# Kernel tuning notes

Measured on AMD Instinct MI355X. Metric: run time of the kernel, lower is better.

Reference implementation:

```python
import jax, jax.numpy as jnp
import numpy as np

W_IMG = 512
H_IMG = 512
D_MODEL = 192
N_FREQ = 8
LN_EPS = 1e-5


def _fourier_pe(coords_norm):
    # coords_norm: [B,K,2] in [0,1); returns [B,K,4*N_FREQ]
    freqs = 2.0 ** jnp.arange(N_FREQ, dtype=jnp.float32)  # [F]
    two_pi = 2.0 * jnp.pi
    x = coords_norm[..., 0:1] * freqs * two_pi  # [B,K,F]
    y = coords_norm[..., 1:2] * freqs * two_pi
    return jnp.concatenate([jnp.sin(x), jnp.cos(x), jnp.sin(y), jnp.cos(y)], axis=-1)


def _bilinear_sample(feat, gx, gy):
    # feat: [B,C,H,W]; gx,gy: [B,K] normalized coords in [-1,1], align_corners=True
    B, C, H, W = feat.shape
    ix = (gx + 1.0) * 0.5 * (W - 1)
    iy = (gy + 1.0) * 0.5 * (H - 1)
    ix0 = jnp.floor(ix)
    iy0 = jnp.floor(iy)
    wx = ix - ix0  # [B,K]
    wy = iy - iy0
    x0 = jnp.clip(ix0.astype(jnp.int32), 0, W - 1)
    x1 = jnp.clip(ix0.astype(jnp.int32) + 1, 0, W - 1)
    y0 = jnp.clip(iy0.astype(jnp.int32), 0, H - 1)
    y1 = jnp.clip(iy0.astype(jnp.int32) + 1, 0, H - 1)
    b = jnp.arange(B)[:, None]  # [B,1] broadcast against [B,K]
    g = lambda y, x: feat[b, :, y, x]  # [B,K,C]
    out = (g(y0, x0) * ((1 - wx) * (1 - wy))[..., None]
           + g(y0, x1) * (wx * (1 - wy))[..., None]
           + g(y1, x0) * ((1 - wx) * wy)[..., None]
           + g(y1, x1) * (wx * wy)[..., None])
    return out  # [B,K,C]


def setup_inputs() -> dict:
    key = jax.random.key(0)
    ks = jax.random.split(key, 16)
    B, K = 8, 4096
    # pixel coordinates in [0, W_IMG-1] x [0, H_IMG-1]
    u = jax.random.uniform(ks[0], (B, K, 2), dtype=jnp.float32)
    coords = u * jnp.array([W_IMG - 1, H_IMG - 1], dtype=jnp.float32)
    L1 = jax.random.normal(ks[1], (B, D_MODEL, 128, 128), dtype=jnp.float32)
    L2 = jax.random.normal(ks[2], (B, D_MODEL, 64, 64), dtype=jnp.float32)
    L3 = jax.random.normal(ks[3], (B, D_MODEL, 32, 32), dtype=jnp.float32)
    L4 = jax.random.normal(ks[4], (B, D_MODEL, 16, 16), dtype=jnp.float32)
    d_in = D_MODEL * 4 + 4 * N_FREQ  # 800
    Wseed_w = jax.random.normal(ks[5], (D_MODEL, d_in), dtype=jnp.float32) / np.sqrt(d_in)
    Wseed_b = jnp.zeros((D_MODEL,), dtype=jnp.float32)
    ln_g = jnp.ones((D_MODEL,), dtype=jnp.float32)
    ln_b = jnp.zeros((D_MODEL,), dtype=jnp.float32)
    Wpos_w = jax.random.normal(ks[6], (D_MODEL, 4 * N_FREQ), dtype=jnp.float32) / np.sqrt(4 * N_FREQ)
    Wpos_b = jnp.zeros((D_MODEL,), dtype=jnp.float32)
    return {"coords": coords, "L1": L1, "L2": L2, "L3": L3, "L4": L4,
            "Wseed_w": Wseed_w, "Wseed_b": Wseed_b, "ln_g": ln_g, "ln_b": ln_b,
            "Wpos_w": Wpos_w, "Wpos_b": Wpos_b}


def reference(coords, L1, L2, L3, L4, Wseed_w, Wseed_b, ln_g, ln_b, Wpos_w, Wpos_b):
    B, K, _ = coords.shape
    # normalized grid in [-1,1] (x uses W, y uses H), align_corners=True convention
    gx = 2.0 * coords[..., 0] / (W_IMG - 1) - 1.0  # [B,K]
    gy = 2.0 * coords[..., 1] / (H_IMG - 1) - 1.0
    center_grid = jnp.stack([gx, gy], axis=-1).reshape(B, K, 1, 2)
    coords_norm = coords / jnp.array([W_IMG, H_IMG], dtype=jnp.float32)
    pe_q = _fourier_pe(coords_norm)  # [B,K,32]
    f1 = _bilinear_sample(L1, gx, gy)
    f2 = _bilinear_sample(L2, gx, gy)
    f3 = _bilinear_sample(L3, gx, gy)
    f4 = _bilinear_sample(L4, gx, gy)
    x = jnp.concatenate([f1, f2, f3, f4, pe_q], axis=-1)  # [B,K,800]
    seed = x @ Wseed_w.T + Wseed_b
    mu = jnp.mean(seed, axis=-1, keepdims=True)
    var = jnp.mean((seed - mu) ** 2, axis=-1, keepdims=True)
    seed = (seed - mu) / jnp.sqrt(var + LN_EPS) * ln_g + ln_b
    pos = pe_q @ Wpos_w.T + Wpos_b
    return (seed, pos, center_grid)
```

## Files before the change

kernel.cpp:

```cpp
#include <hip/hip_runtime.h>
#include <stdint.h>

typedef unsigned short u16;
typedef short s16x8 __attribute__((ext_vector_type(8)));
typedef float f32x4 __attribute__((ext_vector_type(4)));

__device__ __forceinline__ u16 f2bf(float f) {
  union { float f; uint32_t u; } a; a.f = f;
  uint32_t u = a.u;
  uint32_t r = (u + 0x7fffu + ((u >> 16) & 1u)) >> 16;
  return (u16)r;
}
__device__ __forceinline__ float bf2f(uint32_t hbits) {
  union { uint32_t u; float f; } a; a.u = hbits << 16;
  return a.f;
}

__global__ void convert_w_kernel(const float* __restrict__ ws_w,
                                 const float* __restrict__ wp_w,
                                 u16* __restrict__ dst_ws, u16* __restrict__ dst_wp) {
  int i = blockIdx.x * 256 + threadIdx.x;
  if (i < 153600) dst_ws[i] = f2bf(ws_w[i]);
  if (i < 6144)   dst_wp[i] = f2bf(wp_w[i]);
}

__global__ __launch_bounds__(256) void transpose_kernel(const float* __restrict__ src,
                                                        u16* __restrict__ dst, int HW) {
  __shared__ u16 tile[192][66];
  const int b = blockIdx.y;
  const int hw0 = blockIdx.x * 64;
  const int t = threadIdx.x;
  const float* s = src + (size_t)b * 192 * HW + hw0;
  for (int i = 0; i < 48; ++i) {
    int idx = i * 256 + t;
    int c = idx >> 6, hw = idx & 63;
    tile[c][hw] = f2bf(s[(size_t)c * HW + hw]);
  }
  __syncthreads();
  uint32_t* d = (uint32_t*)(dst + ((size_t)b * HW + hw0) * 192);
  for (int i = 0; i < 24; ++i) {
    int e = i * 256 + t;
    int hw = e / 96, c2 = e - hw * 96;
    uint32_t v = (uint32_t)tile[c2 * 2][hw] | ((uint32_t)tile[c2 * 2 + 1][hw] << 16);
    d[hw * 96 + c2] = v;
  }
}

__global__ __launch_bounds__(256, 2) void seed_main(
    const float* __restrict__ coords,
    const u16* __restrict__ T1, const u16* __restrict__ T2,
    const u16* __restrict__ T3, const u16* __restrict__ T4,
    const u16* __restrict__ Wseed, const u16* __restrict__ Wpos,
    const float* __restrict__ seed_b, const float* __restrict__ ln_g,
    const float* __restrict__ ln_b, const float* __restrict__ pos_b,
    float* __restrict__ out_seed, float* __restrict__ out_pos,
    float* __restrict__ out_cg) {

  __shared__ __align__(16) u16 xt[32 * 808];
  __shared__ int   coff[32][4][4];
  __shared__ float cw[32][4][4];
  __shared__ float mu_s[32], rs_s[32];

  const int t = threadIdx.x;
  const int gp0 = blockIdx.x * 32;
  const int b = gp0 >> 12;

  if (t < 128) {
    int p = t >> 2, lv = t & 3;
    float cx = coords[(gp0 + p) * 2 + 0];
    float cy = coords[(gp0 + p) * 2 + 1];
    float gx = 2.0f * cx / 511.0f - 1.0f;
    float gy = 2.0f * cy / 511.0f - 1.0f;
    if (lv == 0) {
      out_cg[(gp0 + p) * 2 + 0] = gx;
      out_cg[(gp0 + p) * 2 + 1] = gy;
    }
    int Wl = 128 >> lv;
    float ix = (gx + 1.0f) * 0.5f * (float)(Wl - 1);
    float iy = (gy + 1.0f) * 0.5f * (float)(Wl - 1);
    float fx = floorf(ix), fy = floorf(iy);
    float wx = ix - fx, wy = iy - fy;
    int x0 = (int)fx, y0 = (int)fy;
    int x1 = x0 + 1, y1 = y0 + 1;
    x0 = min(max(x0, 0), Wl - 1); x1 = min(max(x1, 0), Wl - 1);
    y0 = min(max(y0, 0), Wl - 1); y1 = min(max(y1, 0), Wl - 1);
    coff[p][lv][0] = (y0 * Wl + x0) * 192;
    coff[p][lv][1] = (y0 * Wl + x1) * 192;
    coff[p][lv][2] = (y1 * Wl + x0) * 192;
    coff[p][lv][3] = (y1 * Wl + x1) * 192;
    cw[p][lv][0] = (1.0f - wx) * (1.0f - wy);
    cw[p][lv][1] = wx * (1.0f - wy);
    cw[p][lv][2] = (1.0f - wx) * wy;
    cw[p][lv][3] = wx * wy;
  }
  for (int i = 0; i < 4; ++i) {
    int e = i * 256 + t;
    int p = e >> 5, j = e & 31;
    float c = coords[(gp0 + p) * 2 + ((j >> 4) & 1)] * (1.0f / 512.0f);
    float v = c * (float)(1 << (j & 7));
    float a = (v - floorf(v)) * 6.283185307179586f;
    float r = (j & 8) ? cosf(a) : sinf(a);
    xt[p * 808 + 768 + j] = f2bf(r);
  }
  __syncthreads();

  const size_t psz1 = (size_t)16384 * 192, psz2 = (size_t)4096 * 192,
               psz3 = (size_t)1024 * 192,  psz4 = (size_t)256 * 192;
  const u16* B1 = T1 + (size_t)b * psz1;
  const u16* B2 = T2 + (size_t)b * psz2;
  const u16* B3 = T3 + (size_t)b * psz3;
  const u16* B4 = T4 + (size_t)b * psz4;
  for (int i = 0; i < 48; ++i) {
    int e = i * 256 + t;
    int c2 = e % 96;
    int plv = e / 96;
    int lv = plv & 3, p = plv >> 2;
    const u16* base = (lv == 0) ? B1 : (lv == 1) ? B2 : (lv == 2) ? B3 : B4;
    float w0 = cw[p][lv][0], w1 = cw[p][lv][1], w2 = cw[p][lv][2], w3 = cw[p][lv][3];
    int cc = c2 * 2;
    uint32_t u0 = *(const uint32_t*)(base + coff[p][lv][0] + cc);
    uint32_t u1 = *(const uint32_t*)(base + coff[p][lv][1] + cc);
    uint32_t u2 = *(const uint32_t*)(base + coff[p][lv][2] + cc);
    uint32_t u3 = *(const uint32_t*)(base + coff[p][lv][3] + cc);
    float lo = bf2f(u0 & 0xffff) * w0 + bf2f(u1 & 0xffff) * w1 +
               bf2f(u2 & 0xffff) * w2 + bf2f(u3 & 0xffff) * w3;
    float hi = bf2f(u0 >> 16) * w0 + bf2f(u1 >> 16) * w1 +
               bf2f(u2 >> 16) * w2 + bf2f(u3 >> 16) * w3;
    uint32_t pv = (uint32_t)f2bf(lo) | ((uint32_t)f2bf(hi) << 16);
    *(uint32_t*)(xt + p * 808 + lv * 192 + cc) = pv;
  }
  __syncthreads();

  const int wv = t >> 6, lid = t & 63;
  const int quad = lid >> 4, mrow = lid & 15;
  const int nt0 = wv * 3;

  f32x4 accS[2][3], accP[2][3];
#pragma unroll
  for (int mt = 0; mt < 2; ++mt)
#pragma unroll
    for (int j = 0; j < 3; ++j) { accS[mt][j] = (f32x4)0.0f; accP[mt][j] = (f32x4)0.0f; }

  s16x8 a_last[2];
#pragma unroll 1
  for (int kc = 0; kc < 25; ++kc) {
    int ko = kc * 32 + quad * 8;
    s16x8 a0 = *(const s16x8*)(xt + mrow * 808 + ko);
    s16x8 a1 = *(const s16x8*)(xt + (16 + mrow) * 808 + ko);
#pragma unroll
    for (int j = 0; j < 3; ++j) {
      int n = (nt0 + j) * 16 + mrow;
      s16x8 bw = *(const s16x8*)(Wseed + n * 800 + ko);
      accS[0][j] = __builtin_amdgcn_mfma_f32_16x16x32_bf16(a0, bw, accS[0][j], 0, 0, 0);
      accS[1][j] = __builtin_amdgcn_mfma_f32_16x16x32_bf16(a1, bw, accS[1][j], 0, 0, 0);
    }
    if (kc == 24) { a_last[0] = a0; a_last[1] = a1; }
  }
#pragma unroll
  for (int j = 0; j < 3; ++j) {
    int n = (nt0 + j) * 16 + mrow;
    s16x8 bw = *(const s16x8*)(Wpos + n * 32 + quad * 8);
    accP[0][j] = __builtin_amdgcn_mfma_f32_16x16x32_bf16(a_last[0], bw, accP[0][j], 0, 0, 0);
    accP[1][j] = __builtin_amdgcn_mfma_f32_16x16x32_bf16(a_last[1], bw, accP[1][j], 0, 0, 0);
  }

#pragma unroll
  for (int j = 0; j < 3; ++j) {
    int n = (nt0 + j) * 16 + mrow;
    float pb = pos_b[n];
#pragma unroll
    for (int mt = 0; mt < 2; ++mt)
#pragma unroll
      for (int r = 0; r < 4; ++r) {
        int row = gp0 + mt * 16 + quad * 4 + r;
        out_pos[(size_t)row * 192 + n] = accP[mt][j][r] + pb;
      }
  }

  __syncthreads();
  float* preLN = (float*)xt;
#pragma unroll
  for (int j = 0; j < 3; ++j) {
    int n = (nt0 + j) * 16 + mrow;
    float sb = seed_b[n];
#pragma unroll
    for (int mt = 0; mt < 2; ++mt)
#pragma unroll
      for (int r = 0; r < 4; ++r)
        preLN[(mt * 16 + quad * 4 + r) * 193 + n] = accS[mt][j][r] + sb;
  }
  __syncthreads();

  {
    int r = t >> 3, g = t & 7;
    float s = 0.0f, sq = 0.0f;
    for (int i = 0; i < 24; ++i) {
      float v = preLN[r * 193 + g * 24 + i];
      s += v; sq += v * v;
    }
    for (int d = 4; d > 0; d >>= 1) {
      s += __shfl_down(s, d, 8);
      sq += __shfl_down(sq, d, 8);
    }
    if (g == 0) {
      float mu = s * (1.0f / 192.0f);
      float var = sq * (1.0f / 192.0f) - mu * mu;
      mu_s[r] = mu;
      rs_s[r] = 1.0f / sqrtf(var + 1e-5f);
    }
  }
  __syncthreads();

  for (int i = 0; i < 24; ++i) {
    int e = i * 256 + t;
    int r = e / 192, n = e - r * 192;
    float v = (preLN[r * 193 + n] - mu_s[r]) * rs_s[r] * ln_g[n] + ln_b[n];
    out_seed[(size_t)(gp0 + r) * 192 + n] = v;
  }
}

extern "C" void kernel_launch(void* const* d_in, const int* in_sizes, int n_in,
                              void* d_out, int out_size, void* d_ws, size_t ws_size,
                              hipStream_t stream) {
  const float* coords  = (const float*)d_in[0];
  const float* L1      = (const float*)d_in[1];
  const float* L2      = (const float*)d_in[2];
  const float* L3      = (const float*)d_in[3];
  const float* L4      = (const float*)d_in[4];
  const float* Wseed_w = (const float*)d_in[5];
  const float* Wseed_b = (const float*)d_in[6];
  const float* ln_g    = (const float*)d_in[7];
  const float* ln_b    = (const float*)d_in[8];
  const float* Wpos_w  = (const float*)d_in[9];
  const float* Wpos_b  = (const float*)d_in[10];

  u16* T1  = (u16*)d_ws;
  u16* T2  = T1 + (size_t)8 * 16384 * 192;
  u16* T3  = T2 + (size_t)8 * 4096 * 192;
  u16* T4  = T3 + (size_t)8 * 1024 * 192;
  u16* Wsd = T4 + (size_t)8 * 256 * 192;
  u16* Wps = Wsd + 153600;

  convert_w_kernel<<<600, 256, 0, stream>>>(Wseed_w, Wpos_w, Wsd, Wps);
  transpose_kernel<<<dim3(256, 8), 256, 0, stream>>>(L1, T1, 16384);
  transpose_kernel<<<dim3(64, 8),  256, 0, stream>>>(L2, T2, 4096);
  transpose_kernel<<<dim3(16, 8),  256, 0, stream>>>(L3, T3, 1024);
  transpose_kernel<<<dim3(4, 8),   256, 0, stream>>>(L4, T4, 256);

  float* out_seed = (float*)d_out;
  float* out_pos  = out_seed + (size_t)32768 * 192;
  float* out_cg   = out_pos  + (size_t)32768 * 192;

  seed_main<<<1024, 256, 0, stream>>>(coords, T1, T2, T3, T4, Wsd, Wps,
                                      Wseed_b, ln_g, ln_b, Wpos_b,
                                      out_seed, out_pos, out_cg);
}
```

Before: 307.5 us.

## Fuse prep kernels, vectorize transposes and gathers, shrink seed tiles to 16 points

```diff
diff --git a/kernel.cpp b/kernel.cpp
--- a/kernel.cpp
+++ b/kernel.cpp
@@ -4,6 +4,7 @@
 typedef unsigned short u16;
 typedef short s16x8 __attribute__((ext_vector_type(8)));
 typedef float f32x4 __attribute__((ext_vector_type(4)));
+typedef uint32_t u32x4 __attribute__((ext_vector_type(4)));
 
 __device__ __forceinline__ u16 f2bf(float f) {
   union { float f; uint32_t u; } a; a.f = f;
@@ -16,37 +17,61 @@
   return a.f;
 }
 
-__global__ void convert_w_kernel(const float* __restrict__ ws_w,
-                                 const float* __restrict__ wp_w,
-                                 u16* __restrict__ dst_ws, u16* __restrict__ dst_wp) {
-  int i = blockIdx.x * 256 + threadIdx.x;
-  if (i < 153600) dst_ws[i] = f2bf(ws_w[i]);
-  if (i < 6144)   dst_wp[i] = f2bf(wp_w[i]);
-}
-
-__global__ __launch_bounds__(256) void transpose_kernel(const float* __restrict__ src,
-                                                        u16* __restrict__ dst, int HW) {
-  __shared__ u16 tile[192][66];
-  const int b = blockIdx.y;
-  const int hw0 = blockIdx.x * 64;
+__global__ __launch_bounds__(256) void prep_all(
+    const float* __restrict__ L1, const float* __restrict__ L2,
+    const float* __restrict__ L3, const float* __restrict__ L4,
+    const float* __restrict__ ws_w, const float* __restrict__ wp_w,
+    u16* __restrict__ T1, u16* __restrict__ T2,
+    u16* __restrict__ T3, u16* __restrict__ T4,
+    u16* __restrict__ dWs, u16* __restrict__ dWp) {
+  const int bid = blockIdx.x;
   const int t = threadIdx.x;
-  const float* s = src + (size_t)b * 192 * HW + hw0;
-  for (int i = 0; i < 48; ++i) {
+
+  if (bid >= 2720) {
+    int t0 = (bid - 2720) * 256 + t;
+    for (int i = t0; i < 39936; i += 8192) {
+      const float* s; u16* d; int off;
+      if (i < 38400) { s = ws_w; d = dWs; off = 4 * i; }
+      else           { s = wp_w; d = dWp; off = 4 * (i - 38400); }
+      f32x4 v = *(const f32x4*)(s + off);
+      uint2 o;
+      o.x = (uint32_t)f2bf(v.x) | ((uint32_t)f2bf(v.y) << 16);
+      o.y = (uint32_t)f2bf(v.z) | ((uint32_t)f2bf(v.w) << 16);
+      *(uint2*)(d + off) = o;
+    }
+    return;
+  }
+
+  const float* src; u16* dst; int HW, tiles, rel;
+  if (bid < 2048)      { src = L1; dst = T1; HW = 16384; tiles = 256; rel = bid; }
+  else if (bid < 2560) { src = L2; dst = T2; HW = 4096;  tiles = 64;  rel = bid - 2048; }
+  else if (bid < 2688) { src = L3; dst = T3; HW = 1024;  tiles = 16;  rel = bid - 2560; }
+  else                 { src = L4; dst = T4; HW = 256;   tiles = 4;   rel = bid - 2688; }
+  const int b = rel / tiles, hw0 = (rel % tiles) * 64;
+
+  __shared__ uint32_t tileD[96 * 65];
+  const float* sb = src + (size_t)b * 192 * HW + hw0;
+  for (int i = 0; i < 6; ++i) {
     int idx = i * 256 + t;
-    int c = idx >> 6, hw = idx & 63;
-    tile[c][hw] = f2bf(s[(size_t)c * HW + hw]);
+    int c2 = idx >> 4, hw4 = idx & 15;
+    f32x4 a = *(const f32x4*)(sb + (size_t)(2 * c2) * HW + hw4 * 4);
+    f32x4 c = *(const f32x4*)(sb + (size_t)(2 * c2 + 1) * HW + hw4 * 4);
+    uint32_t* w = &tileD[c2 * 65 + hw4 * 4];
+    w[0] = (uint32_t)f2bf(a.x) | ((uint32_t)f2bf(c.x) << 16);
+    w[1] = (uint32_t)f2bf(a.y) | ((uint32_t)f2bf(c.y) << 16);
+    w[2] = (uint32_t)f2bf(a.z) | ((uint32_t)f2bf(c.z) << 16);
+    w[3] = (uint32_t)f2bf(a.w) | ((uint32_t)f2bf(c.w) << 16);
   }
   __syncthreads();
   uint32_t* d = (uint32_t*)(dst + ((size_t)b * HW + hw0) * 192);
   for (int i = 0; i < 24; ++i) {
     int e = i * 256 + t;
     int hw = e / 96, c2 = e - hw * 96;
-    uint32_t v = (uint32_t)tile[c2 * 2][hw] | ((uint32_t)tile[c2 * 2 + 1][hw] << 16);
-    d[hw * 96 + c2] = v;
-  }
-}
-
-__global__ __launch_bounds__(256, 2) void seed_main(
+    d[hw * 96 + c2] = tileD[c2 * 65 + hw];
+  }
+}
+
+__global__ __launch_bounds__(256, 5) void seed_main(
     const float* __restrict__ coords,
     const u16* __restrict__ T1, const u16* __restrict__ T2,
     const u16* __restrict__ T3, const u16* __restrict__ T4,
@@ -56,112 +81,96 @@
     float* __restrict__ out_seed, float* __restrict__ out_pos,
     float* __restrict__ out_cg) {
 
-  __shared__ __align__(16) u16 xt[32 * 808];
-  __shared__ int   coff[32][4][4];
-  __shared__ float cw[32][4][4];
-  __shared__ float mu_s[32], rs_s[32];
+  __shared__ __align__(16) u16 xt[16 * 808];
+  __shared__ float mu_s[16], rs_s[16];
 
   const int t = threadIdx.x;
-  const int gp0 = blockIdx.x * 32;
+  const int gp0 = blockIdx.x * 16;
   const int b = gp0 >> 12;
 
-  if (t < 128) {
-    int p = t >> 2, lv = t & 3;
+  if (t < 32) {
+    int p = t >> 1, xy = t & 1;
+    float c = coords[(gp0 + p) * 2 + xy];
+    out_cg[(gp0 + p) * 2 + xy] = c * (2.0f / 511.0f) - 1.0f;
+  }
+  for (int i = 0; i < 2; ++i) {
+    int e = i * 256 + t;
+    int p = e >> 5, j = e & 31;
+    float c = coords[(gp0 + p) * 2 + ((j >> 4) & 1)] * (1.0f / 512.0f);
+    float v = c * (float)(1 << (j & 7));
+    float a = (v - floorf(v)) * 6.283185307179586f;
+    float r = (j & 8) ? __cosf(a) : __sinf(a);
+    xt[p * 808 + 768 + j] = f2bf(r);
+  }
+
+  const u16* B1 = T1 + (size_t)b * 16384 * 192;
+  const u16* B2 = T2 + (size_t)b * 4096 * 192;
+  const u16* B3 = T3 + (size_t)b * 1024 * 192;
+  const u16* B4 = T4 + (size_t)b * 256 * 192;
+  for (int i = 0; i < 6; ++i) {
+    int e = i * 256 + t;
+    int c4 = e % 24;
+    int plv = e / 24;
+    int lv = plv & 3, p = plv >> 2;
     float cx = coords[(gp0 + p) * 2 + 0];
     float cy = coords[(gp0 + p) * 2 + 1];
-    float gx = 2.0f * cx / 511.0f - 1.0f;
-    float gy = 2.0f * cy / 511.0f - 1.0f;
-    if (lv == 0) {
-      out_cg[(gp0 + p) * 2 + 0] = gx;
-      out_cg[(gp0 + p) * 2 + 1] = gy;
-    }
+    float gx = cx * (2.0f / 511.0f) - 1.0f;
+    float gy = cy * (2.0f / 511.0f) - 1.0f;
     int Wl = 128 >> lv;
     float ix = (gx + 1.0f) * 0.5f * (float)(Wl - 1);
     float iy = (gy + 1.0f) * 0.5f * (float)(Wl - 1);
     float fx = floorf(ix), fy = floorf(iy);
     float wx = ix - fx, wy = iy - fy;
     int x0 = (int)fx, y0 = (int)fy;
-    int x1 = x0 + 1, y1 = y0 + 1;
-    x0 = min(max(x0, 0), Wl - 1); x1 = min(max(x1, 0), Wl - 1);
-    y0 = min(max(y0, 0), Wl - 1); y1 = min(max(y1, 0), Wl - 1);
-    coff[p][lv][0] = (y0 * Wl + x0) * 192;
-    coff[p][lv][1] = (y0 * Wl + x1) * 192;
-    coff[p][lv][2] = (y1 * Wl + x0) * 192;
-    coff[p][lv][3] = (y1 * Wl + x1) * 192;
-    cw[p][lv][0] = (1.0f - wx) * (1.0f - wy);
-    cw[p][lv][1] = wx * (1.0f - wy);
-    cw[p][lv][2] = (1.0f - wx) * wy;
-    cw[p][lv][3] = wx * wy;
-  }
-  for (int i = 0; i < 4; ++i) {
-    int e = i * 256 + t;
-    int p = e >> 5, j = e & 31;
-    float c = coords[(gp0 + p) * 2 + ((j >> 4) & 1)] * (1.0f / 512.0f);
-    float v = c * (float)(1 << (j & 7));
-    float a = (v - floorf(v)) * 6.283185307179586f;
-    float r = (j & 8) ? cosf(a) : sinf(a);
-    xt[p * 808 + 768 + j] = f2bf(r);
-  }
-  __syncthreads();
-
-  const size_t psz1 = (size_t)16384 * 192, psz2 = (size_t)4096 * 192,
-               psz3 = (size_t)1024 * 192,  psz4 = (size_t)256 * 192;
-  const u16* B1 = T1 + (size_t)b * psz1;
-  const u16* B2 = T2 + (size_t)b * psz2;
-  const u16* B3 = T3 + (size_t)b * psz3;
-  const u16* B4 = T4 + (size_t)b * psz4;
-  for (int i = 0; i < 48; ++i) {
-    int e = i * 256 + t;
-    int c2 = e % 96;
-    int plv = e / 96;
-    int lv = plv & 3, p = plv >> 2;
+    int x1 = min(max(x0 + 1, 0), Wl - 1), y1 = min(max(y0 + 1, 0), Wl - 1);
+    x0 = min(max(x0, 0), Wl - 1); y0 = min(max(y0, 0), Wl - 1);
     const u16* base = (lv == 0) ? B1 : (lv == 1) ? B2 : (lv == 2) ? B3 : B4;
-    float w0 = cw[p][lv][0], w1 = cw[p][lv][1], w2 = cw[p][lv][2], w3 = cw[p][lv][3];
-    int cc = c2 * 2;
-    uint32_t u0 = *(const uint32_t*)(base + coff[p][lv][0] + cc);
-    uint32_t u1 = *(const uint32_t*)(base + coff[p][lv][1] + cc);
-    uint32_t u2 = *(const uint32_t*)(base + coff[p][lv][2] + cc);
-    uint32_t u3 = *(const uint32_t*)(base + coff[p][lv][3] + cc);
-    float lo = bf2f(u0 & 0xffff) * w0 + bf2f(u1 & 0xffff) * w1 +
-               bf2f(u2 & 0xffff) * w2 + bf2f(u3 & 0xffff) * w3;
-    float hi = bf2f(u0 >> 16) * w0 + bf2f(u1 >> 16) * w1 +
-               bf2f(u2 >> 16) * w2 + bf2f(u3 >> 16) * w3;
-    uint32_t pv = (uint32_t)f2bf(lo) | ((uint32_t)f2bf(hi) << 16);
-    *(uint32_t*)(xt + p * 808 + lv * 192 + cc) = pv;
-  }
-  __syncthreads();
-
-  const int wv = t >> 6, lid = t & 63;
+    int cc = c4 * 8;
+    u32x4 q00 = *(const u32x4*)(base + (y0 * Wl + x0) * 192 + cc);
+    u32x4 q01 = *(const u32x4*)(base + (y0 * Wl + x1) * 192 + cc);
+    u32x4 q10 = *(const u32x4*)(base + (y1 * Wl + x0) * 192 + cc);
+    u32x4 q11 = *(const u32x4*)(base + (y1 * Wl + x1) * 192 + cc);
+    float w00 = (1.0f - wx) * (1.0f - wy), w01 = wx * (1.0f - wy);
+    float w10 = (1.0f - wx) * wy,          w11 = wx * wy;
+    u32x4 o;
+#pragma unroll
+    for (int k = 0; k < 4; ++k) {
+      float lo = bf2f(q00[k] & 0xffff) * w00 + bf2f(q01[k] & 0xffff) * w01 +
+                 bf2f(q10[k] & 0xffff) * w10 + bf2f(q11[k] & 0xffff) * w11;
+      float hi = bf2f(q00[k] >> 16) * w00 + bf2f(q01[k] >> 16) * w01 +
+                 bf2f(q10[k] >> 16) * w10 + bf2f(q11[k] >> 16) * w11;
+      o[k] = (uint32_t)f2bf(lo) | ((uint32_t)f2bf(hi) << 16);
+    }
+    *(u32x4*)(xt + p * 808 + lv * 192 + cc) = o;
+  }
+  __syncthreads();
+
+  const int lid = t & 63, wv = t >> 6;
   const int quad = lid >> 4, mrow = lid & 15;
   const int nt0 = wv * 3;
 
-  f32x4 accS[2][3], accP[2][3];
-#pragma unroll
-  for (int mt = 0; mt < 2; ++mt)
-#pragma unroll
-    for (int j = 0; j < 3; ++j) { accS[mt][j] = (f32x4)0.0f; accP[mt][j] = (f32x4)0.0f; }
-
-  s16x8 a_last[2];
+  f32x4 accS[3], accP[3];
+#pragma unroll
+  for (int j = 0; j < 3; ++j) { accS[j] = (f32x4)0.0f; accP[j] = (f32x4)0.0f; }
+
+  s16x8 a_last;
 #pragma unroll 1
   for (int kc = 0; kc < 25; ++kc) {
     int ko = kc * 32 + quad * 8;
-    s16x8 a0 = *(const s16x8*)(xt + mrow * 808 + ko);
-    s16x8 a1 = *(const s16x8*)(xt + (16 + mrow) * 808 + ko);
+    s16x8 a = *(const s16x8*)(xt + mrow * 808 + ko);
 #pragma unroll
     for (int j = 0; j < 3; ++j) {
       int n = (nt0 + j) * 16 + mrow;
       s16x8 bw = *(const s16x8*)(Wseed + n * 800 + ko);
-      accS[0][j] = __builtin_amdgcn_mfma_f32_16x16x32_bf16(a0, bw, accS[0][j], 0, 0, 0);
-      accS[1][j] = __builtin_amdgcn_mfma_f32_16x16x32_bf16(a1, bw, accS[1][j], 0, 0, 0);
-    }
-    if (kc == 24) { a_last[0] = a0; a_last[1] = a1; }
+      accS[j] = __builtin_amdgcn_mfma_f32_16x16x32_bf16(a, bw, accS[j], 0, 0, 0);
+    }
+    if (kc == 24) a_last = a;
   }
 #pragma unroll
   for (int j = 0; j < 3; ++j) {
     int n = (nt0 + j) * 16 + mrow;
     s16x8 bw = *(const s16x8*)(Wpos + n * 32 + quad * 8);
-    accP[0][j] = __builtin_amdgcn_mfma_f32_16x16x32_bf16(a_last[0], bw, accP[0][j], 0, 0, 0);
-    accP[1][j] = __builtin_amdgcn_mfma_f32_16x16x32_bf16(a_last[1], bw, accP[1][j], 0, 0, 0);
+    accP[j] = __builtin_amdgcn_mfma_f32_16x16x32_bf16(a_last, bw, accP[j], 0, 0, 0);
   }
 
 #pragma unroll
@@ -169,12 +178,8 @@
     int n = (nt0 + j) * 16 + mrow;
     float pb = pos_b[n];
 #pragma unroll
-    for (int mt = 0; mt < 2; ++mt)
-#pragma unroll
-      for (int r = 0; r < 4; ++r) {
-        int row = gp0 + mt * 16 + quad * 4 + r;
-        out_pos[(size_t)row * 192 + n] = accP[mt][j][r] + pb;
-      }
+    for (int r = 0; r < 4; ++r)
+      out_pos[(size_t)(gp0 + quad * 4 + r) * 192 + n] = accP[j][r] + pb;
   }
 
   __syncthreads();
@@ -184,23 +189,23 @@
     int n = (nt0 + j) * 16 + mrow;
     float sb = seed_b[n];
 #pragma unroll
-    for (int mt = 0; mt < 2; ++mt)
-#pragma unroll
-      for (int r = 0; r < 4; ++r)
-        preLN[(mt * 16 + quad * 4 + r) * 193 + n] = accS[mt][j][r] + sb;
+    for (int r = 0; r < 4; ++r)
+      preLN[(quad * 4 + r) * 193 + n] = accS[j][r] + sb;
   }
   __syncthreads();
 
   {
-    int r = t >> 3, g = t & 7;
+    int r = t >> 4, g = t & 15;
     float s = 0.0f, sq = 0.0f;
-    for (int i = 0; i < 24; ++i) {
-      float v = preLN[r * 193 + g * 24 + i];
+#pragma unroll
+    for (int i = 0; i < 12; ++i) {
+      float v = preLN[r * 193 + g * 12 + i];
       s += v; sq += v * v;
     }
-    for (int d = 4; d > 0; d >>= 1) {
-      s += __shfl_down(s, d, 8);
-      sq += __shfl_down(sq, d, 8);
+#pragma unroll
+    for (int d = 8; d > 0; d >>= 1) {
+      s += __shfl_down(s, d, 16);
+      sq += __shfl_down(sq, d, 16);
     }
     if (g == 0) {
       float mu = s * (1.0f / 192.0f);
@@ -211,7 +216,7 @@
   }
   __syncthreads();
 
-  for (int i = 0; i < 24; ++i) {
+  for (int i = 0; i < 12; ++i) {
     int e = i * 256 + t;
     int r = e / 192, n = e - r * 192;
     float v = (preLN[r * 193 + n] - mu_s[r]) * rs_s[r] * ln_g[n] + ln_b[n];
@@ -241,17 +246,14 @@
   u16* Wsd = T4 + (size_t)8 * 256 * 192;
   u16* Wps = Wsd + 153600;
 
-  convert_w_kernel<<<600, 256, 0, stream>>>(Wseed_w, Wpos_w, Wsd, Wps);
-  transpose_kernel<<<dim3(256, 8), 256, 0, stream>>>(L1, T1, 16384);
-  transpose_kernel<<<dim3(64, 8),  256, 0, stream>>>(L2, T2, 4096);
-  transpose_kernel<<<dim3(16, 8),  256, 0, stream>>>(L3, T3, 1024);
-  transpose_kernel<<<dim3(4, 8),   256, 0, stream>>>(L4, T4, 256);
+  prep_all<<<2752, 256, 0, stream>>>(L1, L2, L3, L4, Wseed_w, Wpos_w,
+                                     T1, T2, T3, T4, Wsd, Wps);
 
   float* out_seed = (float*)d_out;
   float* out_pos  = out_seed + (size_t)32768 * 192;
   float* out_cg   = out_pos  + (size_t)32768 * 192;
 
-  seed_main<<<1024, 256, 0, stream>>>(coords, T1, T2, T3, T4, Wsd, Wps,
+  seed_main<<<2048, 256, 0, stream>>>(coords, T1, T2, T3, T4, Wsd, Wps,
                                       Wseed_b, ln_g, ln_b, Wpos_b,
                                       out_seed, out_pos, out_cg);
 }
```

Result: faster. 278.0 us (-9.6%).
